# Kernel optimization log

Hardware: AMD Instinct MI355X
Metric: run time of the kernel (lower is better)

## Reference

```python
import jax, jax.numpy as jnp
import numpy as np

T = 543  # fixed sequence length implied by dense1 = Linear(543*64, 64)


def gru_layer(x, w_ih, w_hh, b_ih, b_hh):
    """PyTorch-convention GRU over x:[B,T,I]. Gate order: r, z, n."""
    B = x.shape[0]
    H = w_hh.shape[1]
    # Precompute input contributions for all timesteps in one GEMM: [B,T,3H]
    xg = jnp.einsum('bti,gi->btg', x, w_ih) + b_ih

    def step(h, xg_t):
        hg = h @ w_hh.T + b_hh  # [B,3H]
        xr, xz, xn = jnp.split(xg_t, 3, axis=-1)
        hr, hz, hn = jnp.split(hg, 3, axis=-1)
        r = jax.nn.sigmoid(xr + hr)
        z = jax.nn.sigmoid(xz + hz)
        n = jnp.tanh(xn + r * hn)
        h_new = (1.0 - z) * n + z * h
        return h_new, h_new

    h0 = jnp.zeros((B, H), x.dtype)
    _, hs = jax.lax.scan(step, h0, jnp.swapaxes(xg, 0, 1))  # [T,B,H]
    return jnp.swapaxes(hs, 0, 1)  # [B,T,H]


def _gru_params(key, in_dim, hidden):
    k1, k2, k3, k4 = jax.random.split(key, 4)
    s = 1.0 / np.sqrt(hidden)
    return (
        jax.random.uniform(k1, (3 * hidden, in_dim), jnp.float32, -s, s),
        jax.random.uniform(k2, (3 * hidden, hidden), jnp.float32, -s, s),
        jax.random.uniform(k3, (3 * hidden,), jnp.float32, -s, s),
        jax.random.uniform(k4, (3 * hidden,), jnp.float32, -s, s),
    )


def _linear_params(key, in_dim, out_dim):
    k1, k2 = jax.random.split(key)
    s = 1.0 / np.sqrt(in_dim)
    return (
        jax.random.uniform(k1, (out_dim, in_dim), jnp.float32, -s, s),
        jax.random.uniform(k2, (out_dim,), jnp.float32, -s, s),
    )


def setup_inputs() -> dict:
    key = jax.random.key(0)
    keys = jax.random.split(key, 8)
    B, input_size = 2048, 3
    x = jax.random.normal(keys[0], (B, T, input_size), jnp.float32)
    w_ih1, w_hh1, b_ih1, b_hh1 = _gru_params(keys[1], input_size, 64)
    w_ih2, w_hh2, b_ih2, b_hh2 = _gru_params(keys[2], 64, 128)
    w_ih3, w_hh3, b_ih3, b_hh3 = _gru_params(keys[3], 128, 64)
    w1, bd1 = _linear_params(keys[4], T * 64, 64)
    w2, bd2 = _linear_params(keys[5], 64, 32)
    w3, bd3 = _linear_params(keys[6], 32, 250)
    return dict(x=x,
                w_ih1=w_ih1, w_hh1=w_hh1, b_ih1=b_ih1, b_hh1=b_hh1,
                w_ih2=w_ih2, w_hh2=w_hh2, b_ih2=b_ih2, b_hh2=b_hh2,
                w_ih3=w_ih3, w_hh3=w_hh3, b_ih3=b_ih3, b_hh3=b_hh3,
                w1=w1, bd1=bd1, w2=w2, bd2=bd2, w3=w3, bd3=bd3)


def reference(x,
              w_ih1, w_hh1, b_ih1, b_hh1,
              w_ih2, w_hh2, b_ih2, b_hh2,
              w_ih3, w_hh3, b_ih3, b_hh3,
              w1, bd1, w2, bd2, w3, bd3):
    h = jax.nn.relu(gru_layer(x, w_ih1, w_hh1, b_ih1, b_hh1))
    h = jax.nn.relu(gru_layer(h, w_ih2, w_hh2, b_ih2, b_hh2))
    h = jax.nn.relu(gru_layer(h, w_ih3, w_hh3, b_ih3, b_hh3))
    h = h.reshape(h.shape[0], -1)  # [B, 543*64]
    h = jax.nn.relu(h @ w1.T + bd1)
    h = jax.nn.relu(h @ w2.T + bd2)
    h = jax.nn.relu(h @ w3.T + bd3)
    return h
```

## Files before the change

### kernel.cpp

```cpp
#include <hip/hip_runtime.h>

#define T_SEQ 543
#define B_TOT 2048

typedef _Float16 f16;
typedef f16   f16x8 __attribute__((ext_vector_type(8)));
typedef f16   f16x2 __attribute__((ext_vector_type(2)));
typedef float f32x4 __attribute__((ext_vector_type(4)));

#if defined(__has_builtin)
#if __has_builtin(__builtin_amdgcn_rcpf)
#define RCP(x) __builtin_amdgcn_rcpf(x)
#endif
#endif
#ifndef RCP
#define RCP(x) (1.0f / (x))
#endif

__device__ __forceinline__ float sigm(float x)   { return RCP(1.0f + __expf(-x)); }
__device__ __forceinline__ float tanh_f(float x) { return fmaf(-2.0f, RCP(__expf(2.0f * x) + 1.0f), 1.0f); }

__device__ __forceinline__ f32x4 mfma16(f16x8 a, f16x8 b, f32x4 c) {
    return __builtin_amdgcn_mfma_f32_16x16x32_f16(a, b, c, 0, 0, 0);
}

__device__ __forceinline__ f16x8 loadB(const float* __restrict__ g, int nrow, int ldk, int k0) {
    const float* p = g + (size_t)nrow * ldk + k0;
    float4 a = *(const float4*)p;
    float4 b = *(const float4*)(p + 4);
    f16x8 r;
    r[0] = (f16)a.x; r[1] = (f16)a.y; r[2] = (f16)a.z; r[3] = (f16)a.w;
    r[4] = (f16)b.x; r[5] = (f16)b.y; r[6] = (f16)b.z; r[7] = (f16)b.w;
    return r;
}

#define L_H1S 0
#define L_H2S 4096
#define L_H3S 12288
#define L_H1R 16384
#define L_H2R 18432
#define L_H3R 22528
#define L_X1  26624
#define L_W1D 26880
#define SMEM_T 43264

__device__ __forceinline__ f16x8 ldsA(const unsigned char* sm, int base, int stride, int row, int kByte) {
    int off = (base + row * stride + kByte) ^ ((row & 7) << 4);
    return *(const f16x8*)(sm + off);
}
__device__ __forceinline__ void stH(unsigned char* sm, int base, int stride, int row, int col, f16 v) {
    int off = (base + row * stride + col * 2) ^ ((row & 7) << 4);
    *(f16*)(sm + off) = v;
}

__global__ void cvt_f16(const float* __restrict__ s, f16* __restrict__ d, int n) {
    int i = blockIdx.x * 256 + threadIdx.x;
    if (i < n) d[i] = (f16)s[i];
}

__device__ __forceinline__ float gru_cell(float aR, float aZ, float aXn, float aHn, float hprev) {
    float r = sigm(aR);
    float z = sigm(aZ);
    float n = tanh_f(aXn + r * aHn);
    return fmaf(z, hprev - n, n);
}

template<bool W1H>
__global__ __launch_bounds__(512, 2) void gru_fused(
    const float* __restrict__ x,
    const float* __restrict__ w_ih1, const float* __restrict__ w_hh1,
    const float* __restrict__ b_ih1, const float* __restrict__ b_hh1,
    const float* __restrict__ w_ih2, const float* __restrict__ w_hh2,
    const float* __restrict__ b_ih2, const float* __restrict__ b_hh2,
    const float* __restrict__ w_ih3, const float* __restrict__ w_hh3,
    const float* __restrict__ b_ih3, const float* __restrict__ b_hh3,
    const f16* __restrict__ w1h, const float* __restrict__ w1, const float* __restrict__ bd1,
    const float* __restrict__ w2, const float* __restrict__ bd2,
    const float* __restrict__ w3, const float* __restrict__ bd3,
    float* __restrict__ out)
{
    __shared__ __align__(16) unsigned char sm[SMEM_T];
    const int tid = threadIdx.x;
    const int Bb  = blockIdx.x * 8;
    const int wv  = tid >> 6;
    const int l   = tid & 63;
    const int lc  = l & 15;
    const int lr  = l >> 4;

    for (int e = tid * 4; e < SMEM_T; e += 512 * 4) *(float*)(sm + e) = 0.0f;
    if (tid < 24) {
        int row = tid / 3, c = tid - row * 3;
        *(float*)(sm + L_X1 + row * 32 + c * 4) = x[(size_t)(Bb + row) * T_SEQ * 3 + c];
    }

    f16x8 b1h[3][2];
    f16x8 b3x[3][4], b3h[3][2];
    f16x8 b2x[3][2], b2h[3][4];
    float wi1[9];
    float bs1r = 0, bs1z = 0, bi1n = 0, bh1n = 0;
    float bs3r = 0, bs3z = 0, bi3n = 0, bh3n = 0;

    const int cj = (wv & 3) * 16 + lc;
    if (wv < 4) {
        #pragma unroll
        for (int g = 0; g < 3; ++g)
            #pragma unroll
            for (int kt = 0; kt < 2; ++kt)
                b1h[g][kt] = loadB(w_hh1, g * 64 + cj, 64, kt * 32 + lr * 8);
        bs1r = b_ih1[cj] + b_hh1[cj];
        bs1z = b_ih1[cj + 64] + b_hh1[cj + 64];
        bi1n = b_ih1[cj + 128]; bh1n = b_hh1[cj + 128];
        #pragma unroll
        for (int g = 0; g < 3; ++g)
            #pragma unroll
            for (int i = 0; i < 3; ++i) wi1[g * 3 + i] = w_ih1[(cj + g * 64) * 3 + i];
    } else {
        #pragma unroll
        for (int g = 0; g < 3; ++g) {
            #pragma unroll
            for (int kt = 0; kt < 4; ++kt)
                b3x[g][kt] = loadB(w_ih3, g * 64 + cj, 128, kt * 32 + lr * 8);
            #pragma unroll
            for (int kt = 0; kt < 2; ++kt)
                b3h[g][kt] = loadB(w_hh3, g * 64 + cj, 64, kt * 32 + lr * 8);
        }
        bs3r = b_ih3[cj] + b_hh3[cj];
        bs3z = b_ih3[cj + 64] + b_hh3[cj + 64];
        bi3n = b_ih3[cj + 128]; bh3n = b_hh3[cj + 128];
    }
    const int cj2 = wv * 16 + lc;
    #pragma unroll
    for (int g = 0; g < 3; ++g) {
        #pragma unroll
        for (int kt = 0; kt < 2; ++kt)
            b2x[g][kt] = loadB(w_ih2, g * 128 + cj2, 64, kt * 32 + lr * 8);
        #pragma unroll
        for (int kt = 0; kt < 4; ++kt)
            b2h[g][kt] = loadB(w_hh2, g * 128 + cj2, 128, kt * 32 + lr * 8);
    }
    const float bs2r = b_ih2[cj2] + b_hh2[cj2];
    const float bs2z = b_ih2[cj2 + 128] + b_hh2[cj2 + 128];
    const float bi2n = b_ih2[cj2 + 256], bh2n = b_hh2[cj2 + 256];

    float h1own[2] = {0, 0}, h2own[2] = {0, 0}, h3own[2] = {0, 0};
    f32x4 accd4 = {0, 0, 0, 0};

    const int sjo = tid >> 3;
    const int skq = (tid & 7) ^ (sjo & 7);
    const size_t ssrc = (size_t)sjo * (T_SEQ * 64);

    __syncthreads();

    #pragma unroll 1
    for (int t = 0; t <= T_SEQ + 1; ++t) {
        f16x8 wstage;
        const int ts = t - 1;
        const bool doStage = (t >= 1) && (ts < T_SEQ);
        if (doStage) {
            if constexpr (W1H) {
                wstage = *(const f16x8*)(w1h + ssrc + (size_t)ts * 64 + skq * 8);
            } else {
                const float* p = w1 + ssrc + (size_t)ts * 64 + skq * 8;
                float4 a = *(const float4*)p, b = *(const float4*)(p + 4);
                wstage[0] = (f16)a.x; wstage[1] = (f16)a.y; wstage[2] = (f16)a.z; wstage[3] = (f16)a.w;
                wstage[4] = (f16)b.x; wstage[5] = (f16)b.y; wstage[6] = (f16)b.z; wstage[7] = (f16)b.w;
            }
        }

        if (wv < 4) {
            if (t < T_SEQ) {
                const int curO = ((t + 1) & 1) * 2048, nxtO = (t & 1) * 2048;
                f16x8 ah0 = ldsA(sm, L_H1S + curO, 128, lc, lr * 16);
                f16x8 ah1 = ldsA(sm, L_H1S + curO, 128, lc, 64 + lr * 16);
                f32x4 aR = {bs1r, bs1r, bs1r, bs1r};
                f32x4 aZ = {bs1z, bs1z, bs1z, bs1z};
                f32x4 aN = {bh1n, bh1n, bh1n, bh1n};
                __builtin_amdgcn_s_setprio(1);
                aR = mfma16(ah0, b1h[0][0], aR); aR = mfma16(ah1, b1h[0][1], aR);
                aZ = mfma16(ah0, b1h[1][0], aZ); aZ = mfma16(ah1, b1h[1][1], aZ);
                aN = mfma16(ah0, b1h[2][0], aN); aN = mfma16(ah1, b1h[2][1], aN);
                __builtin_amdgcn_s_setprio(0);
                #pragma unroll
                for (int ii = 0; ii < 2; ++ii) {
                    const int i = ii * 2, row = lr * 4 + i;
                    float4 xv = *(const float4*)(sm + L_X1 + row * 16);
                    float xgr = wi1[0] * xv.x + wi1[1] * xv.y + wi1[2] * xv.z;
                    float xgz = wi1[3] * xv.x + wi1[4] * xv.y + wi1[5] * xv.z;
                    float xgn = wi1[6] * xv.x + wi1[7] * xv.y + wi1[8] * xv.z;
                    h1own[ii] = gru_cell(aR[i] + xgr, aZ[i] + xgz, xgn + bi1n, aN[i], h1own[ii]);
                    stH(sm, L_H1S + nxtO, 128, row, cj, (f16)h1own[ii]);
                    stH(sm, L_H1R, 128, row, cj, (f16)fmaxf(h1own[ii], 0.f));
                }
            }
            if (t >= 2) {
                const int ts2 = t - 2;
                f16x8 dh0 = ldsA(sm, L_H3R + (t & 1) * 2048, 128, lc, lr * 16);
                f16x8 dh1 = ldsA(sm, L_H3R + (t & 1) * 2048, 128, lc, 64 + lr * 16);
                const unsigned char* wb = sm + L_W1D + (ts2 & 1) * 8192 + cj * 128;
                f16x8 wb0 = *(const f16x8*)(wb + ((lr ^ (cj & 7)) << 4));
                f16x8 wb1 = *(const f16x8*)(wb + (((4 + lr) ^ (cj & 7)) << 4));
                accd4 = mfma16(dh0, wb0, accd4);
                accd4 = mfma16(dh1, wb1, accd4);
            }
        } else {
            if (t >= 1 && t <= T_SEQ) {
                const int curO = (t & 1) * 2048, nxtO = ((t + 1) & 1) * 2048;
                f16x8 ax0 = ldsA(sm, L_H2R, 256, lc, lr * 16);
                f16x8 ax1 = ldsA(sm, L_H2R, 256, lc, 64 + lr * 16);
                f16x8 ax2 = ldsA(sm, L_H2R, 256, lc, 128 + lr * 16);
                f16x8 ax3 = ldsA(sm, L_H2R, 256, lc, 192 + lr * 16);
                f16x8 ah0 = ldsA(sm, L_H3S + curO, 128, lc, lr * 16);
                f16x8 ah1 = ldsA(sm, L_H3S + curO, 128, lc, 64 + lr * 16);
                f32x4 aR  = {bs3r, bs3r, bs3r, bs3r};
                f32x4 aZ  = {bs3z, bs3z, bs3z, bs3z};
                f32x4 aXn = {bi3n, bi3n, bi3n, bi3n};
                f32x4 aHn = {bh3n, bh3n, bh3n, bh3n};
                __builtin_amdgcn_s_setprio(1);
                aR = mfma16(ax0, b3x[0][0], aR); aR = mfma16(ax1, b3x[0][1], aR);
                aR = mfma16(ax2, b3x[0][2], aR); aR = mfma16(ax3, b3x[0][3], aR);
                aR = mfma16(ah0, b3h[0][0], aR); aR = mfma16(ah1, b3h[0][1], aR);
                aZ = mfma16(ax0, b3x[1][0], aZ); aZ = mfma16(ax1, b3x[1][1], aZ);
                aZ = mfma16(ax2, b3x[1][2], aZ); aZ = mfma16(ax3, b3x[1][3], aZ);
                aZ = mfma16(ah0, b3h[1][0], aZ); aZ = mfma16(ah1, b3h[1][1], aZ);
                aXn = mfma16(ax0, b3x[2][0], aXn); aXn = mfma16(ax1, b3x[2][1], aXn);
                aXn = mfma16(ax2, b3x[2][2], aXn); aXn = mfma16(ax3, b3x[2][3], aXn);
                aHn = mfma16(ah0, b3h[2][0], aHn); aHn = mfma16(ah1, b3h[2][1], aHn);
                __builtin_amdgcn_s_setprio(0);
                #pragma unroll
                for (int ii = 0; ii < 2; ++ii) {
                    const int i = ii * 2, row = lr * 4 + i;
                    h3own[ii] = gru_cell(aR[i], aZ[i], aXn[i], aHn[i], h3own[ii]);
                    stH(sm, L_H3S + nxtO, 128, row, cj, (f16)h3own[ii]);
                    stH(sm, L_H3R + nxtO, 128, row, cj, (f16)fmaxf(h3own[ii], 0.f));
                }
            }
        }
        if (doStage)
            *(f16x8*)(sm + L_W1D + (ts & 1) * 8192 + tid * 16) = wstage;
        __syncthreads();

        if (t < T_SEQ) {
            const int curO = ((t + 1) & 1) * 4096, nxtO = (t & 1) * 4096;
            f16x8 ax0 = ldsA(sm, L_H1R, 128, lc, lr * 16);
            f16x8 ax1 = ldsA(sm, L_H1R, 128, lc, 64 + lr * 16);
            f16x8 ah0 = ldsA(sm, L_H2S + curO, 256, lc, lr * 16);
            f16x8 ah1 = ldsA(sm, L_H2S + curO, 256, lc, 64 + lr * 16);
            f16x8 ah2 = ldsA(sm, L_H2S + curO, 256, lc, 128 + lr * 16);
            f16x8 ah3 = ldsA(sm, L_H2S + curO, 256, lc, 192 + lr * 16);
            f32x4 aR  = {bs2r, bs2r, bs2r, bs2r};
            f32x4 aZ  = {bs2z, bs2z, bs2z, bs2z};
            f32x4 aXn = {bi2n, bi2n, bi2n, bi2n};
            f32x4 aHn = {bh2n, bh2n, bh2n, bh2n};
            __builtin_amdgcn_s_setprio(1);
            aR = mfma16(ax0, b2x[0][0], aR); aR = mfma16(ax1, b2x[0][1], aR);
            aR = mfma16(ah0, b2h[0][0], aR); aR = mfma16(ah1, b2h[0][1], aR);
            aR = mfma16(ah2, b2h[0][2], aR); aR = mfma16(ah3, b2h[0][3], aR);
            aZ = mfma16(ax0, b2x[1][0], aZ); aZ = mfma16(ax1, b2x[1][1], aZ);
            aZ = mfma16(ah0, b2h[1][0], aZ); aZ = mfma16(ah1, b2h[1][1], aZ);
            aZ = mfma16(ah2, b2h[1][2], aZ); aZ = mfma16(ah3, b2h[1][3], aZ);
            aXn = mfma16(ax0, b2x[2][0], aXn); aXn = mfma16(ax1, b2x[2][1], aXn);
            aHn = mfma16(ah0, b2h[2][0], aHn); aHn = mfma16(ah1, b2h[2][1], aHn);
            aHn = mfma16(ah2, b2h[2][2], aHn); aHn = mfma16(ah3, b2h[2][3], aHn);
            __builtin_amdgcn_s_setprio(0);
            #pragma unroll
            for (int ii = 0; ii < 2; ++ii) {
                const int i = ii * 2, row = lr * 4 + i;
                h2own[ii] = gru_cell(aR[i], aZ[i], aXn[i], aHn[i], h2own[ii]);
                stH(sm, L_H2S + nxtO, 256, row, cj2, (f16)h2own[ii]);
                stH(sm, L_H2R, 256, row, cj2, (f16)fmaxf(h2own[ii], 0.f));
            }
        }
        if (wv < 4 && t + 1 < T_SEQ && tid < 24) {
            int row = tid / 3, c = tid - row * 3;
            *(float*)(sm + L_X1 + row * 32 + c * 4) =
                x[(size_t)(Bb + row) * T_SEQ * 3 + (size_t)(t + 1) * 3 + c];
        }
        __syncthreads();
    }

    float* o1 = (float*)sm;
    if (wv < 4) {
        #pragma unroll
        for (int ii = 0; ii < 2; ++ii) {
            const int row = lr * 4 + ii * 2;
            o1[(row >> 1) * 68 + cj] = fmaxf(accd4[ii * 2] + bd1[cj], 0.f);
        }
    }
    __syncthreads();
    float* o2 = (float*)(sm + 4096);
    if (tid < 256) {
        const int bb = tid & 7, m = tid >> 3;
        float acc = bd2[m];
        const float* w2p = w2 + m * 64;
        const float* o1q = o1 + bb * 68;
        #pragma unroll
        for (int i = 0; i < 16; ++i) {
            float4 a = *(const float4*)(o1q + i * 4);
            float4 wv8 = *(const float4*)(w2p + i * 4);
            acc += a.x * wv8.x + a.y * wv8.y + a.z * wv8.z + a.w * wv8.w;
        }
        o2[bb * 36 + m] = fmaxf(acc, 0.f);
    }
    __syncthreads();
    for (int e = tid; e < 8 * 250; e += 512) {
        const int bb = e / 250, p = e - bb * 250;
        float acc = bd3[p];
        const float* w3p = w3 + p * 32;
        const float* o2p = o2 + bb * 36;
        #pragma unroll
        for (int i = 0; i < 8; ++i) {
            float4 a = *(const float4*)(o2p + i * 4);
            float4 wv8 = *(const float4*)(w3p + i * 4);
            acc += a.x * wv8.x + a.y * wv8.y + a.z * wv8.z + a.w * wv8.w;
        }
        out[(size_t)(Bb + bb) * 250 + p] = fmaxf(acc, 0.f);
    }
}

extern "C" void kernel_launch(void* const* d_in, const int* in_sizes, int n_in,
                              void* d_out, int out_size, void* d_ws, size_t ws_size,
                              hipStream_t stream) {
    const float* x     = (const float*)d_in[0];
    const float* w_ih1 = (const float*)d_in[1];
    const float* w_hh1 = (const float*)d_in[2];
    const float* b_ih1 = (const float*)d_in[3];
    const float* b_hh1 = (const float*)d_in[4];
    const float* w_ih2 = (const float*)d_in[5];
    const float* w_hh2 = (const float*)d_in[6];
    const float* b_ih2 = (const float*)d_in[7];
    const float* b_hh2 = (const float*)d_in[8];
    const float* w_ih3 = (const float*)d_in[9];
    const float* w_hh3 = (const float*)d_in[10];
    const float* b_ih3 = (const float*)d_in[11];
    const float* b_hh3 = (const float*)d_in[12];
    const float* w1    = (const float*)d_in[13];
    const float* bd1   = (const float*)d_in[14];
    const float* w2    = (const float*)d_in[15];
    const float* bd2   = (const float*)d_in[16];
    const float* w3    = (const float*)d_in[17];
    const float* bd3   = (const float*)d_in[18];
    float* out = (float*)d_out;

    const int n1 = 64 * T_SEQ * 64;
    const bool useF16 = ws_size >= (size_t)n1 * sizeof(f16);
    f16* w1h = (f16*)d_ws;

    if (useF16) {
        hipLaunchKernelGGL(cvt_f16, dim3((n1 + 255) / 256), dim3(256), 0, stream, w1, w1h, n1);
        hipLaunchKernelGGL((gru_fused<true>), dim3(B_TOT / 8), dim3(512), 0, stream,
                           x, w_ih1, w_hh1, b_ih1, b_hh1, w_ih2, w_hh2, b_ih2, b_hh2,
                           w_ih3, w_hh3, b_ih3, b_hh3,
                           w1h, w1, bd1, w2, bd2, w3, bd3, out);
    } else {
        hipLaunchKernelGGL((gru_fused<false>), dim3(B_TOT / 8), dim3(512), 0, stream,
                           x, w_ih1, w_hh1, b_ih1, b_hh1, w_ih2, w_hh2, b_ih2, b_hh2,
                           w_ih3, w_hh3, b_ih3, b_hh3,
                           w1h, w1, bd1, w2, bd2, w3, bd3, out);
    }
}
```

Before: 1.448 ms.

## Skew GRU layer pipeline to one barrier per timestep with double-buffered activations

Restructures the fused three-layer GRU wavefront so that layer 2 runs one step behind layer 1 and layer 3 two steps behind. All inter-layer activation buffers, the x input, and the staged dense weights are double-buffered by step parity. This removes the mid-iteration __syncthreads, leaving one barrier per step instead of two. The cost is more LDS and one extra pipeline iteration. Layer 2 now executes concurrently with layers 1 and 3 instead of after a barrier.

```diff
diff --git a/kernel.cpp b/kernel.cpp
--- a/kernel.cpp
+++ b/kernel.cpp
@@ -5,7 +5,6 @@
 
 typedef _Float16 f16;
 typedef f16   f16x8 __attribute__((ext_vector_type(8)));
-typedef f16   f16x2 __attribute__((ext_vector_type(2)));
 typedef float f32x4 __attribute__((ext_vector_type(4)));
 
 #if defined(__has_builtin)
@@ -35,14 +34,14 @@
 }
 
 #define L_H1S 0
-#define L_H2S 4096
-#define L_H3S 12288
-#define L_H1R 16384
-#define L_H2R 18432
-#define L_H3R 22528
-#define L_X1  26624
-#define L_W1D 26880
-#define SMEM_T 43264
+#define L_H1R 4096
+#define L_H2S 8192
+#define L_H2R 16384
+#define L_H3S 24576
+#define L_H3R 28672
+#define L_X1  32768
+#define L_W1D 33280
+#define SMEM_T 49664
 
 __device__ __forceinline__ f16x8 ldsA(const unsigned char* sm, int base, int stride, int row, int kByte) {
     int off = (base + row * stride + kByte) ^ ((row & 7) << 4);
@@ -152,10 +151,12 @@
     __syncthreads();
 
     #pragma unroll 1
-    for (int t = 0; t <= T_SEQ + 1; ++t) {
+    for (int t = 0; t <= T_SEQ + 2; ++t) {
+        const int pe = t & 1, po = (t + 1) & 1;
+
         f16x8 wstage;
-        const int ts = t - 1;
-        const bool doStage = (t >= 1) && (ts < T_SEQ);
+        const int ts = t - 2;
+        const bool doStage = (ts >= 0) && (ts < T_SEQ);
         if (doStage) {
             if constexpr (W1H) {
                 wstage = *(const f16x8*)(w1h + ssrc + (size_t)ts * 64 + skq * 8);
@@ -169,9 +170,8 @@
 
         if (wv < 4) {
             if (t < T_SEQ) {
-                const int curO = ((t + 1) & 1) * 2048, nxtO = (t & 1) * 2048;
-                f16x8 ah0 = ldsA(sm, L_H1S + curO, 128, lc, lr * 16);
-                f16x8 ah1 = ldsA(sm, L_H1S + curO, 128, lc, 64 + lr * 16);
+                f16x8 ah0 = ldsA(sm, L_H1S + po * 2048, 128, lc, lr * 16);
+                f16x8 ah1 = ldsA(sm, L_H1S + po * 2048, 128, lc, 64 + lr * 16);
                 f32x4 aR = {bs1r, bs1r, bs1r, bs1r};
                 f32x4 aZ = {bs1z, bs1z, bs1z, bs1z};
                 f32x4 aN = {bh1n, bh1n, bh1n, bh1n};
@@ -183,34 +183,23 @@
                 #pragma unroll
                 for (int ii = 0; ii < 2; ++ii) {
                     const int i = ii * 2, row = lr * 4 + i;
-                    float4 xv = *(const float4*)(sm + L_X1 + row * 16);
+                    float4 xv = *(const float4*)(sm + L_X1 + pe * 256 + row * 16);
                     float xgr = wi1[0] * xv.x + wi1[1] * xv.y + wi1[2] * xv.z;
                     float xgz = wi1[3] * xv.x + wi1[4] * xv.y + wi1[5] * xv.z;
                     float xgn = wi1[6] * xv.x + wi1[7] * xv.y + wi1[8] * xv.z;
                     h1own[ii] = gru_cell(aR[i] + xgr, aZ[i] + xgz, xgn + bi1n, aN[i], h1own[ii]);
-                    stH(sm, L_H1S + nxtO, 128, row, cj, (f16)h1own[ii]);
-                    stH(sm, L_H1R, 128, row, cj, (f16)fmaxf(h1own[ii], 0.f));
+                    stH(sm, L_H1S + pe * 2048, 128, row, cj, (f16)h1own[ii]);
+                    stH(sm, L_H1R + pe * 2048, 128, row, cj, (f16)fmaxf(h1own[ii], 0.f));
                 }
             }
-            if (t >= 2) {
-                const int ts2 = t - 2;
-                f16x8 dh0 = ldsA(sm, L_H3R + (t & 1) * 2048, 128, lc, lr * 16);
-                f16x8 dh1 = ldsA(sm, L_H3R + (t & 1) * 2048, 128, lc, 64 + lr * 16);
-                const unsigned char* wb = sm + L_W1D + (ts2 & 1) * 8192 + cj * 128;
-                f16x8 wb0 = *(const f16x8*)(wb + ((lr ^ (cj & 7)) << 4));
-                f16x8 wb1 = *(const f16x8*)(wb + (((4 + lr) ^ (cj & 7)) << 4));
-                accd4 = mfma16(dh0, wb0, accd4);
-                accd4 = mfma16(dh1, wb1, accd4);
-            }
         } else {
-            if (t >= 1 && t <= T_SEQ) {
-                const int curO = (t & 1) * 2048, nxtO = ((t + 1) & 1) * 2048;
-                f16x8 ax0 = ldsA(sm, L_H2R, 256, lc, lr * 16);
-                f16x8 ax1 = ldsA(sm, L_H2R, 256, lc, 64 + lr * 16);
-                f16x8 ax2 = ldsA(sm, L_H2R, 256, lc, 128 + lr * 16);
-                f16x8 ax3 = ldsA(sm, L_H2R, 256, lc, 192 + lr * 16);
-                f16x8 ah0 = ldsA(sm, L_H3S + curO, 128, lc, lr * 16);
-                f16x8 ah1 = ldsA(sm, L_H3S + curO, 128, lc, 64 + lr * 16);
+            if (t >= 2 && t <= T_SEQ + 1) {
+                f16x8 ax0 = ldsA(sm, L_H2R + pe * 4096, 256, lc, lr * 16);
+                f16x8 ax1 = ldsA(sm, L_H2R + pe * 4096, 256, lc, 64 + lr * 16);
+                f16x8 ax2 = ldsA(sm, L_H2R + pe * 4096, 256, lc, 128 + lr * 16);
+                f16x8 ax3 = ldsA(sm, L_H2R + pe * 4096, 256, lc, 192 + lr * 16);
+                f16x8 ah0 = ldsA(sm, L_H3S + po * 2048, 128, lc, lr * 16);
+                f16x8 ah1 = ldsA(sm, L_H3S + po * 2048, 128, lc, 64 + lr * 16);
                 f32x4 aR  = {bs3r, bs3r, bs3r, bs3r};
                 f32x4 aZ  = {bs3z, bs3z, bs3z, bs3z};
                 f32x4 aXn = {bi3n, bi3n, bi3n, bi3n};
@@ -230,23 +219,19 @@
                 for (int ii = 0; ii < 2; ++ii) {
                     const int i = ii * 2, row = lr * 4 + i;
                     h3own[ii] = gru_cell(aR[i], aZ[i], aXn[i], aHn[i], h3own[ii]);
-                    stH(sm, L_H3S + nxtO, 128, row, cj, (f16)h3own[ii]);
-                    stH(sm, L_H3R + nxtO, 128, row, cj, (f16)fmaxf(h3own[ii], 0.f));
+                    stH(sm, L_H3S + pe * 2048, 128, row, cj, (f16)h3own[ii]);
+                    stH(sm, L_H3R + pe * 2048, 128, row, cj, (f16)fmaxf(h3own[ii], 0.f));
                 }
             }
         }
-        if (doStage)
-            *(f16x8*)(sm + L_W1D + (ts & 1) * 8192 + tid * 16) = wstage;
-        __syncthreads();
-
-        if (t < T_SEQ) {
-            const int curO = ((t + 1) & 1) * 4096, nxtO = (t & 1) * 4096;
-            f16x8 ax0 = ldsA(sm, L_H1R, 128, lc, lr * 16);
-            f16x8 ax1 = ldsA(sm, L_H1R, 128, lc, 64 + lr * 16);
-            f16x8 ah0 = ldsA(sm, L_H2S + curO, 256, lc, lr * 16);
-            f16x8 ah1 = ldsA(sm, L_H2S + curO, 256, lc, 64 + lr * 16);
-            f16x8 ah2 = ldsA(sm, L_H2S + curO, 256, lc, 128 + lr * 16);
-            f16x8 ah3 = ldsA(sm, L_H2S + curO, 256, lc, 192 + lr * 16);
+
+        if (t >= 1 && t <= T_SEQ) {
+            f16x8 ax0 = ldsA(sm, L_H1R + po * 2048, 128, lc, lr * 16);
+            f16x8 ax1 = ldsA(sm, L_H1R + po * 2048, 128, lc, 64 + lr * 16);
+            f16x8 ah0 = ldsA(sm, L_H2S + pe * 4096, 256, lc, lr * 16);
+            f16x8 ah1 = ldsA(sm, L_H2S + pe * 4096, 256, lc, 64 + lr * 16);
+            f16x8 ah2 = ldsA(sm, L_H2S + pe * 4096, 256, lc, 128 + lr * 16);
+            f16x8 ah3 = ldsA(sm, L_H2S + pe * 4096, 256, lc, 192 + lr * 16);
             f32x4 aR  = {bs2r, bs2r, bs2r, bs2r};
             f32x4 aZ  = {bs2z, bs2z, bs2z, bs2z};
             f32x4 aXn = {bi2n, bi2n, bi2n, bi2n};
@@ -266,13 +251,26 @@
             for (int ii = 0; ii < 2; ++ii) {
                 const int i = ii * 2, row = lr * 4 + i;
                 h2own[ii] = gru_cell(aR[i], aZ[i], aXn[i], aHn[i], h2own[ii]);
-                stH(sm, L_H2S + nxtO, 256, row, cj2, (f16)h2own[ii]);
-                stH(sm, L_H2R, 256, row, cj2, (f16)fmaxf(h2own[ii], 0.f));
+                stH(sm, L_H2S + po * 4096, 256, row, cj2, (f16)h2own[ii]);
+                stH(sm, L_H2R + po * 4096, 256, row, cj2, (f16)fmaxf(h2own[ii], 0.f));
             }
         }
-        if (wv < 4 && t + 1 < T_SEQ && tid < 24) {
-            int row = tid / 3, c = tid - row * 3;
-            *(float*)(sm + L_X1 + row * 32 + c * 4) =
+
+        if (wv < 4 && t >= 3) {
+            f16x8 dh0 = ldsA(sm, L_H3R + po * 2048, 128, lc, lr * 16);
+            f16x8 dh1 = ldsA(sm, L_H3R + po * 2048, 128, lc, 64 + lr * 16);
+            const unsigned char* wb = sm + L_W1D + po * 8192 + cj * 128;
+            f16x8 wb0 = *(const f16x8*)(wb + ((lr ^ (cj & 7)) << 4));
+            f16x8 wb1 = *(const f16x8*)(wb + (((4 + lr) ^ (cj & 7)) << 4));
+            accd4 = mfma16(dh0, wb0, accd4);
+            accd4 = mfma16(dh1, wb1, accd4);
+        }
+
+        if (doStage)
+            *(f16x8*)(sm + L_W1D + pe * 8192 + tid * 16) = wstage;
+        if (wv >= 4 && t + 1 < T_SEQ && tid < 256 + 24) {
+            int h = tid - 256, row = h / 3, c = h - row * 3;
+            *(float*)(sm + L_X1 + po * 256 + row * 32 + c * 4) =
                 x[(size_t)(Bb + row) * T_SEQ * 3 + (size_t)(t + 1) * 3 + c];
         }
         __syncthreads();
```

New measurement: 1.348 ms, median of 3. 6.9% less time.
